# Kernel tuning notes

Hardware: AMD Instinct MI355X
Metric: run time of the kernel (lower is better)

## Reference

```python
import jax, jax.numpy as jnp
import numpy as np
import math

N, T, D_MODEL, H, D = 4, 2048, 1024, 16, 64


def setup_inputs() -> dict:
    key = jax.random.key(0)
    ks = jax.random.split(key, 12)
    s = 0.02
    return {
        "xq": jax.random.normal(ks[0], (N, T, D_MODEL), dtype=jnp.float32),
        "xk": jax.random.normal(ks[1], (N, T, D_MODEL), dtype=jnp.float32),
        "xv": jax.random.normal(ks[2], (N, T, D_MODEL), dtype=jnp.float32),
        "padding_mask": jnp.ones((N, T), dtype=jnp.int32),
        "Wq": jax.random.normal(ks[3], (D_MODEL, H * D), dtype=jnp.float32) * s,
        "bq": jnp.zeros((H * D,), dtype=jnp.float32),
        "Wk": jax.random.normal(ks[4], (D_MODEL, H * D), dtype=jnp.float32) * s,
        "bk": jnp.zeros((H * D,), dtype=jnp.float32),
        "Wv": jax.random.normal(ks[5], (D_MODEL, H * D), dtype=jnp.float32) * s,
        "bv": jnp.zeros((H * D,), dtype=jnp.float32),
        "Wo": jax.random.normal(ks[6], (H * D, D_MODEL), dtype=jnp.float32) * s,
        "bo": jnp.zeros((D_MODEL,), dtype=jnp.float32),
    }


def reference(xq, xk, xv, padding_mask, Wq, bq, Wk, bk, Wv, bv, Wo, bo):
    n, t_out, _ = xq.shape
    t_in = xk.shape[1]
    # projections
    Q = (xq @ Wq + bq).reshape(n, t_out, H, D).transpose(0, 2, 1, 3)  # [N,H,Tq,D]
    K = (xk @ Wk + bk).reshape(n, t_in, H, D).transpose(0, 2, 1, 3)   # [N,H,Tk,D]
    V = (xv @ Wv + bv).reshape(n, t_in, H, D).transpose(0, 2, 1, 3)
    scores = jnp.einsum("bhqd,bhkd->bhqk", Q, K) / math.sqrt(D)       # [N,H,Tq,Tk]
    neg_inf = jnp.float32(-jnp.inf)
    # padding mask: mask keys where padding_mask == 0
    scores = jnp.where(padding_mask[:, None, None, :] == 0, neg_inf, scores)
    # causal mask (tril of ones[max_len,max_len] sliced to [Tq,Tk])
    q_idx = jnp.arange(t_out)[:, None]
    k_idx = jnp.arange(t_in)[None, :]
    scores = jnp.where((k_idx <= q_idx)[None, None, :, :], scores, neg_inf)
    w = jax.nn.softmax(scores, axis=-1)
    attn = jnp.einsum("bhqk,bhkd->bhqd", w, V)                         # [N,H,Tq,D]
    attn = attn.transpose(0, 2, 1, 3).reshape(n, t_out, H * D)
    return attn @ Wo + bo
```

## Files before the change

### kernel.cpp

```cpp
#include <hip/hip_runtime.h>
#include <hip/hip_bf16.h>
#include <cstdint>

#define NB 4
#define TT 2048
#define DM 1024
#define NH 16
#define HD 64
#define QBLK 256
#define KVB 64

typedef __attribute__((ext_vector_type(8))) short bf16x8;
typedef __attribute__((ext_vector_type(4))) float f32x4;
typedef __attribute__((ext_vector_type(16))) float f32x16;
typedef __attribute__((ext_vector_type(4))) float float4v;
typedef __attribute__((ext_vector_type(4))) int i32x4;

static __device__ __forceinline__ unsigned short f2bf(float x) {
    unsigned int u = __float_as_uint(x);
    unsigned int r = (u + 0x7fffu + ((u >> 16) & 1u)) >> 16;
    return (unsigned short)r;
}
static __device__ __forceinline__ uint32_t pk2bf(float lo, float hi) {
    return (uint32_t)f2bf(lo) | ((uint32_t)f2bf(hi) << 16);
}

#define GLOAD16(gp, lp) __builtin_amdgcn_global_load_lds(                 \
    (const __attribute__((address_space(1))) void*)(gp),                  \
    (__attribute__((address_space(3))) void*)(lp), 16, 0, 0)
#define BAR() asm volatile("s_barrier" ::: "memory")
#define WAITV8() asm volatile("s_waitcnt vmcnt(8)" ::: "memory")
#define WAITV2() asm volatile("s_waitcnt vmcnt(2)" ::: "memory")
#define WAITV0() asm volatile("s_waitcnt vmcnt(0)" ::: "memory")

__global__ __launch_bounds__(256) void k_cvt3(const float* __restrict__ sq,
                                              const float* __restrict__ sk,
                                              const float* __restrict__ sv,
                                              unsigned short* __restrict__ dst,
                                              int n8) {
    const int z = blockIdx.y;
    const float* s = (z == 0) ? sq : (z == 1) ? sk : sv;
    unsigned short* d = dst + (size_t)z * n8 * 8;
    int i = blockIdx.x * 256 + threadIdx.x;
    const int stride = gridDim.x * 256;
    for (; i < n8; i += stride) {
        const float4v* sp = (const float4v*)(s + (size_t)i * 8);
        float4v v0 = sp[0], v1 = sp[1];
        uint4 o;
        o.x = pk2bf(v0[0], v0[1]);
        o.y = pk2bf(v0[2], v0[3]);
        o.z = pk2bf(v1[0], v1[1]);
        o.w = pk2bf(v1[2], v1[3]);
        *(uint4*)(d + (size_t)i * 8) = o;
    }
}

__global__ __launch_bounds__(256) void k_transpose_w(const float* __restrict__ W,
                                                     unsigned short* __restrict__ Wt) {
    __shared__ unsigned short tile[32][33];
    int tx = threadIdx.x, ty = threadIdx.y;
    int kb = blockIdx.x * 32, nb = blockIdx.y * 32;
#pragma unroll
    for (int i = 0; i < 4; ++i)
        tile[ty + i * 8][tx] = f2bf(W[(size_t)(kb + ty + i * 8) * DM + nb + tx]);
    __syncthreads();
#pragma unroll
    for (int i = 0; i < 4; ++i)
        Wt[(size_t)(nb + ty + i * 8) * DM + kb + tx] = tile[tx][ty + i * 8];
}

__global__ __launch_bounds__(256) void k_transpose_v(const unsigned short* __restrict__ V,
                                                     unsigned short* __restrict__ Vt) {
    __shared__ unsigned short tile[32][34];
    int tx = threadIdx.x, ty = threadIdx.y;
    int bh = blockIdx.z;
    int t0 = blockIdx.x * 32, d0 = blockIdx.y * 32;
    const unsigned short* src = V + (size_t)bh * TT * HD;
    unsigned short* dst = Vt + (size_t)bh * HD * TT;
#pragma unroll
    for (int i = 0; i < 4; ++i)
        tile[ty + i * 8][tx] = src[(size_t)(t0 + ty + i * 8) * HD + d0 + tx];
    __syncthreads();
#pragma unroll
    for (int i = 0; i < 4; ++i)
        dst[(size_t)(d0 + ty + i * 8) * TT + t0 + tx] = tile[tx][ty + i * 8];
}

template <int BATCHED>
__global__ __launch_bounds__(256) void k_gemm(const unsigned short* __restrict__ A0,
                                              const unsigned short* __restrict__ Bt0,
                                              const float* __restrict__ bias0,
                                              const float* __restrict__ bias1,
                                              const float* __restrict__ bias2,
                                              void* __restrict__ Cv, float scale0) {
    __shared__ __align__(16) char Asl[2][16384];
    __shared__ __align__(16) char Bsl[2][16384];
    const int tid = threadIdx.x;
    const int lane = tid & 63, wid = tid >> 6;
    const int lg = lane >> 4, lc = lane & 15;
    const int wm = wid >> 1, wn = wid & 1;
    const int m0 = blockIdx.x * 128, n0 = blockIdx.y * 128;
    const int z = BATCHED ? blockIdx.z : 0;

    const char* Ab = (const char*)(A0 + (size_t)z * NB * TT * DM);
    const char* Bb = (const char*)(Bt0 + (size_t)z * DM * DM);
    const float* bias = (z == 0) ? bias0 : (z == 1) ? bias1 : bias2;
    const float scale = (BATCHED && z != 0) ? 1.0f : scale0;

    f32x4 acc[4][4];
#pragma unroll
    for (int mi = 0; mi < 4; ++mi)
#pragma unroll
        for (int ni = 0; ni < 4; ++ni)
            acc[mi][ni] = (f32x4){0.f, 0.f, 0.f, 0.f};

    auto stage = [&](int buf, int k0) {
#pragma unroll
        for (int j = 0; j < 4; ++j) {
            const int row = j * 32 + (tid >> 3);
            const int swz = ((tid & 7) * 16) ^ ((row & 7) << 4);
            GLOAD16(Ab + (size_t)(m0 + row) * (DM * 2) + k0 * 2 + swz,
                    &Asl[buf][0] + j * 4096 + tid * 16);
            GLOAD16(Bb + (size_t)(n0 + row) * (DM * 2) + k0 * 2 + swz,
                    &Bsl[buf][0] + j * 4096 + tid * 16);
        }
    };

    stage(0, 0);
    __syncthreads();

    int cur = 0;
    for (int t = 0; t < DM / 64; ++t) {
        if (t + 1 < DM / 64) {
            stage(cur ^ 1, (t + 1) * 64);
            WAITV8();
        } else {
            WAITV0();
        }
        BAR();

#pragma unroll
        for (int kk = 0; kk < 2; ++kk) {
            bf16x8 af[4], bfr[4];
#pragma unroll
            for (int ni = 0; ni < 4; ++ni) {
                const int n = wn * 64 + ni * 16 + lc;
                bfr[ni] = *(const bf16x8*)(&Bsl[cur][0] + n * 128 +
                                           ((kk * 64 + lg * 16) ^ ((n & 7) << 4)));
            }
#pragma unroll
            for (int mi = 0; mi < 4; ++mi) {
                const int m = wm * 64 + mi * 16 + lc;
                af[mi] = *(const bf16x8*)(&Asl[cur][0] + m * 128 +
                                          ((kk * 64 + lg * 16) ^ ((m & 7) << 4)));
            }
            __builtin_amdgcn_s_setprio(1);
#pragma unroll
            for (int mi = 0; mi < 4; ++mi)
#pragma unroll
                for (int ni = 0; ni < 4; ++ni)
                    acc[mi][ni] = __builtin_amdgcn_mfma_f32_16x16x32_bf16(af[mi], bfr[ni],
                                                                          acc[mi][ni], 0, 0, 0);
            __builtin_amdgcn_s_setprio(0);
        }
        BAR();
        cur ^= 1;
    }

#pragma unroll
    for (int mi = 0; mi < 4; ++mi)
#pragma unroll
        for (int ni = 0; ni < 4; ++ni)
#pragma unroll
            for (int r = 0; r < 4; ++r) {
                int m = m0 + wm * 64 + mi * 16 + lg * 4 + r;
                int n = n0 + wn * 64 + ni * 16 + lc;
                float val = (acc[mi][ni][r] + bias[n]) * scale;
                if (BATCHED) {
                    int b = m >> 11, t = m & (TT - 1), h = n >> 6, d = n & 63;
                    ((unsigned short*)Cv)[(size_t)z * NB * NH * TT * HD +
                                          (((size_t)b * NH + h) * TT + t) * HD + d] = f2bf(val);
                } else {
                    ((float*)Cv)[(size_t)m * DM + n] = val;
                }
            }
}

__global__ __launch_bounds__(512) void k_attn(const unsigned short* __restrict__ Qg,
                                              const unsigned short* __restrict__ Kg,
                                              const unsigned short* __restrict__ Vtg,
                                              const int* __restrict__ pm,
                                              unsigned short* __restrict__ Og) {
    __shared__ __align__(16) unsigned short Kl[2][KVB * HD];
    __shared__ __align__(16) unsigned short Vl[2][KVB * HD];
    __shared__ uint64_t pmbits[TT / 64];

    const int idx = blockIdx.x;
    const int half = idx >> 8, r5 = idx & 255;
    const int a = r5 & 3;
    const int qb = half ? (7 - a) : a;
    const int bh = r5 >> 2;
    const int b = bh >> 4, h = bh & 15;
    const int qbase = qb * QBLK;
    const int tid = threadIdx.x;
    const int wid = tid >> 6, lane = tid & 63;
    const int hi = lane >> 5, l31 = lane & 31;
    const int q0 = qbase + wid * 32;
    const int q = q0 + l31;

    const unsigned short* Qh = Qg + (size_t)bh * TT * HD;
    const char* Khb = (const char*)(Kg + (size_t)bh * TT * HD);
    const char* Vthb = (const char*)(Vtg + (size_t)bh * HD * TT);
    const int* pmb = pm + b * TT;

    char* const kdst = (char*)&Kl[0][0];
    char* const vdst = (char*)&Vl[0][0];

    GLOAD16(Khb + (size_t)lane * 128 + wid * 16, kdst + tid * 16);
    GLOAD16(Vthb + (size_t)lane * 4096 + wid * 16, vdst + tid * 16);

#pragma unroll
    for (int it = 0; it < 4; ++it) {
        const int g = wid + it * 8;
        unsigned long long msk = __ballot(pmb[g * 64 + lane] != 0);
        if (lane == 0) pmbits[g] = msk;
    }

    bf16x8 qf[4];
#pragma unroll
    for (int dd = 0; dd < 4; ++dd)
        qf[dd] = *(const bf16x8*)((const char*)Qh + (size_t)q * 128 + dd * 32 + hi * 16);

    f32x16 o0, o1;
#pragma unroll
    for (int r = 0; r < 16; ++r) { o0[r] = 0.f; o1[r] = 0.f; }
    float mrow = -INFINITY, msafe = -1.0e30f, lrow = 0.f;

    __syncthreads();

    const int nt = (qbase + QBLK) >> 6;
    int cur = 0;
    for (int t = 0; t < nt; ++t) {
        const int kv0 = t << 6;
        if (t + 1 < nt) {
            const int kn = kv0 + KVB;
            const int nb = (cur ^ 1) * 8192 + tid * 16;
            GLOAD16(Khb + (size_t)(kn + lane) * 128 + wid * 16, kdst + nb);
            GLOAD16(Vthb + (size_t)lane * 4096 + (size_t)kn * 2 + wid * 16, vdst + nb);
            WAITV2();
        } else {
            WAITV0();
        }
        BAR();

        if (kv0 <= q0 + 31) {
            const uint64_t vb = pmbits[kv0 >> 6];
            const uint32_t pm0 = ((uint32_t)vb) >> (4 * hi);
            const uint32_t pm1 = ((uint32_t)(vb >> 32)) >> (4 * hi);
            const bool allvalid = (vb == ~0ull);
            const bool do2 = (kv0 + 32 <= q0 + 31);
            const bool needmask = (kv0 + 63 > q0) || !allvalid;
            const char* kb = (const char*)&Kl[0][0] + cur * 8192;
            const char* vbp = (const char*)&Vl[0][0] + cur * 8192;

            f32x16 st0, st1;
#pragma unroll
            for (int r = 0; r < 16; ++r) { st0[r] = 0.f; st1[r] = 0.f; }
            __builtin_amdgcn_s_setprio(1);
#pragma unroll
            for (int dd = 0; dd < 4; ++dd) {
                const char* kchunk = kb + (dd * 2 + hi) * 1024;
                bf16x8 kf = *(const bf16x8*)(kchunk + l31 * 16);
                st0 = __builtin_amdgcn_mfma_f32_32x32x16_bf16(kf, qf[dd], st0, 0, 0, 0);
            }
            if (do2) {
#pragma unroll
                for (int dd = 0; dd < 4; ++dd) {
                    const char* kchunk = kb + (dd * 2 + hi) * 1024;
                    bf16x8 kf = *(const bf16x8*)(kchunk + 512 + l31 * 16);
                    st1 = __builtin_amdgcn_mfma_f32_32x32x16_bf16(kf, qf[dd], st1, 0, 0, 0);
                }
            }
            __builtin_amdgcn_s_setprio(0);

            const int qr = q - kv0 - 4 * hi;
            if (needmask) {
#pragma unroll
                for (int r = 0; r < 16; ++r) {
                    const int c = (r & 3) + 8 * (r >> 2);
                    st0[r] = (((pm0 >> c) & 1) && (c <= qr)) ? st0[r] : -INFINITY;
                }
                if (do2) {
#pragma unroll
                    for (int r = 0; r < 16; ++r) {
                        const int c = (r & 3) + 8 * (r >> 2);
                        st1[r] = (((pm1 >> c) & 1) && (c + 32 <= qr)) ? st1[r] : -INFINITY;
                    }
                }
            }

            float mloc = -INFINITY;
#pragma unroll
            for (int r = 0; r < 16; ++r) mloc = fmaxf(mloc, st0[r]);
            if (do2) {
#pragma unroll
                for (int r = 0; r < 16; ++r) mloc = fmaxf(mloc, st1[r]);
            }
            const float cmax = fmaxf(mloc, __shfl_xor(mloc, 32, 64));
            if (!__all(cmax - mrow <= 8.0f)) {
                const float mnew = fmaxf(mrow, cmax);
                const float ms = fmaxf(mnew, -1.0e30f);
                const float esc = __builtin_amdgcn_exp2f(mrow - ms);
#pragma unroll
                for (int r = 0; r < 16; ++r) { o0[r] *= esc; o1[r] *= esc; }
                lrow *= esc;
                mrow = mnew;
                msafe = ms;
            }

            float tot = 0.f;
#pragma unroll
            for (int r = 0; r < 16; ++r) {
                st0[r] = __builtin_amdgcn_exp2f(st0[r] - msafe);
                tot += st0[r];
            }
            if (do2) {
#pragma unroll
                for (int r = 0; r < 16; ++r) {
                    st1[r] = __builtin_amdgcn_exp2f(st1[r] - msafe);
                    tot += st1[r];
                }
            }
            lrow += tot + __shfl_xor(tot, 32, 64);

            __builtin_amdgcn_s_setprio(1);
#pragma unroll
            for (int kc = 0; kc < 2; ++kc) {
                uint32_t A0 = pk2bf(st0[kc * 8 + 0], st0[kc * 8 + 1]);
                uint32_t A1 = pk2bf(st0[kc * 8 + 2], st0[kc * 8 + 3]);
                uint32_t C0 = pk2bf(st0[kc * 8 + 4], st0[kc * 8 + 5]);
                uint32_t C1 = pk2bf(st0[kc * 8 + 6], st0[kc * 8 + 7]);
                uint32_t oA0 = __shfl_xor(A0, 32, 64), oA1 = __shfl_xor(A1, 32, 64);
                uint32_t oC0 = __shfl_xor(C0, 32, 64), oC1 = __shfl_xor(C1, 32, 64);
                i32x4 pf = {(int)(hi ? oC0 : A0), (int)(hi ? oC1 : A1),
                            (int)(hi ? C0 : oA0), (int)(hi ? C1 : oA1)};
                bf16x8 pb = *(bf16x8*)&pf;
                const char* vchunk = vbp + (kc * 2 + hi) * 1024;
                {
                    bf16x8 vf = *(const bf16x8*)(vchunk + l31 * 16);
                    o0 = __builtin_amdgcn_mfma_f32_32x32x16_bf16(vf, pb, o0, 0, 0, 0);
                }
                {
                    bf16x8 vf = *(const bf16x8*)(vchunk + 512 + l31 * 16);
                    o1 = __builtin_amdgcn_mfma_f32_32x32x16_bf16(vf, pb, o1, 0, 0, 0);
                }
            }
            if (do2) {
#pragma unroll
                for (int kc = 0; kc < 2; ++kc) {
                    uint32_t A0 = pk2bf(st1[kc * 8 + 0], st1[kc * 8 + 1]);
                    uint32_t A1 = pk2bf(st1[kc * 8 + 2], st1[kc * 8 + 3]);
                    uint32_t C0 = pk2bf(st1[kc * 8 + 4], st1[kc * 8 + 5]);
                    uint32_t C1 = pk2bf(st1[kc * 8 + 6], st1[kc * 8 + 7]);
                    uint32_t oA0 = __shfl_xor(A0, 32, 64), oA1 = __shfl_xor(A1, 32, 64);
                    uint32_t oC0 = __shfl_xor(C0, 32, 64), oC1 = __shfl_xor(C1, 32, 64);
                    i32x4 pf = {(int)(hi ? oC0 : A0), (int)(hi ? oC1 : A1),
                                (int)(hi ? C0 : oA0), (int)(hi ? C1 : oA1)};
                    bf16x8 pb = *(bf16x8*)&pf;
                    const char* vchunk = vbp + (4 + kc * 2 + hi) * 1024;
                    {
                        bf16x8 vf = *(const bf16x8*)(vchunk + l31 * 16);
                        o0 = __builtin_amdgcn_mfma_f32_32x32x16_bf16(vf, pb, o0, 0, 0, 0);
                    }
                    {
                        bf16x8 vf = *(const bf16x8*)(vchunk + 512 + l31 * 16);
                        o1 = __builtin_amdgcn_mfma_f32_32x32x16_bf16(vf, pb, o1, 0, 0, 0);
                    }
                }
            }
            __builtin_amdgcn_s_setprio(0);
        }
        BAR();
        cur ^= 1;
    }

    const float inv = (lrow > 0.f) ? (1.0f / lrow) : 0.f;
    unsigned short* orow = Og + ((size_t)(b * TT + q)) * DM + h * HD;
#pragma unroll
    for (int g4 = 0; g4 < 4; ++g4) {
        uint32_t w0 = pk2bf(o0[g4 * 4 + 0] * inv, o0[g4 * 4 + 1] * inv);
        uint32_t w1 = pk2bf(o0[g4 * 4 + 2] * inv, o0[g4 * 4 + 3] * inv);
        *(uint2*)(orow + g4 * 8 + 4 * hi) = make_uint2(w0, w1);
    }
#pragma unroll
    for (int g4 = 0; g4 < 4; ++g4) {
        uint32_t w0 = pk2bf(o1[g4 * 4 + 0] * inv, o1[g4 * 4 + 1] * inv);
        uint32_t w1 = pk2bf(o1[g4 * 4 + 2] * inv, o1[g4 * 4 + 3] * inv);
        *(uint2*)(orow + 32 + g4 * 8 + 4 * hi) = make_uint2(w0, w1);
    }
}

extern "C" void kernel_launch(void* const* d_in, const int* in_sizes, int n_in,
                              void* d_out, int out_size, void* d_ws, size_t ws_size,
                              hipStream_t stream) {
    const float* xq = (const float*)d_in[0];
    const float* xk = (const float*)d_in[1];
    const float* xv = (const float*)d_in[2];
    const int* pmask = (const int*)d_in[3];
    const float* Wq = (const float*)d_in[4];
    const float* bq = (const float*)d_in[5];
    const float* Wk = (const float*)d_in[6];
    const float* bk = (const float*)d_in[7];
    const float* Wv = (const float*)d_in[8];
    const float* bv = (const float*)d_in[9];
    const float* Wo = (const float*)d_in[10];
    const float* bo = (const float*)d_in[11];

    char* ws = (char*)d_ws;
    const size_t WT = (size_t)DM * DM * 2;
    const size_t QKV = (size_t)NB * NH * TT * HD * 2;
    unsigned short* WqT = (unsigned short*)(ws + 0 * WT);
    unsigned short* WoT = (unsigned short*)(ws + 3 * WT);
    unsigned short* Qb = (unsigned short*)(ws + 4 * WT);
    unsigned short* Kb = (unsigned short*)(ws + 4 * WT + QKV);
    unsigned short* Vb = (unsigned short*)(ws + 4 * WT + 2 * QKV);
    unsigned short* Vt = (unsigned short*)(ws + 4 * WT + 3 * QKV);
    unsigned short* Xb = (unsigned short*)(ws + 4 * WT + 4 * QKV);
    unsigned short* Ob = Vb;

    dim3 tb(32, 8);
    k_transpose_w<<<dim3(32, 32), tb, 0, stream>>>(Wq, WqT);
    k_transpose_w<<<dim3(32, 32), tb, 0, stream>>>(Wk, WqT + DM * DM);
    k_transpose_w<<<dim3(32, 32), tb, 0, stream>>>(Wv, WqT + 2 * DM * DM);
    k_transpose_w<<<dim3(32, 32), tb, 0, stream>>>(Wo, WoT);

    const float qscale = 0.125f * 1.44269504088896340736f;
    const int n8 = NB * TT * DM / 8;

    k_cvt3<<<dim3(1024, 3), 256, 0, stream>>>(xq, xk, xv, Xb, n8);
    k_gemm<1><<<dim3(64, 8, 3), 256, 0, stream>>>(Xb, WqT, bq, bk, bv, Qb, qscale);

    k_transpose_v<<<dim3(TT / 32, HD / 32, NB * NH), tb, 0, stream>>>(Vb, Vt);

    k_attn<<<dim3((TT / QBLK) * NB * NH), 512, 0, stream>>>(Qb, Kb, Vt, pmask, Ob);

    k_gemm<0><<<dim3(64, 8, 1), 256, 0, stream>>>(Ob, WoT, bo, bo, bo, d_out, 1.0f);
}
```

Before: 216.6 us.

## Fuse fp32-to-bf16 input conversion and V transpose into QKV projection GEMM

The QKV GEMM now loads fp32 activations directly through registers, converts them to bf16 and writes them into swizzled LDS. This removes the separate conversion kernel and its bf16 round trip through global memory. The V projection epilogue writes straight into the transposed layout, so the separate V transpose kernel is dropped. In exchange the A operand no longer uses async global-to-LDS loads, and register-staged conversion adds VALU work and register pressure inside the GEMM main loop.

```diff
diff --git a/kernel.cpp b/kernel.cpp
--- a/kernel.cpp
+++ b/kernel.cpp
@@ -22,38 +22,20 @@
     return (unsigned short)r;
 }
 static __device__ __forceinline__ uint32_t pk2bf(float lo, float hi) {
-    return (uint32_t)f2bf(lo) | ((uint32_t)f2bf(hi) << 16);
+    union { __hip_bfloat162 v; uint32_t u; } c;
+    c.v = __float22bfloat162_rn(float2{lo, hi});
+    return c.u;
 }
 
 #define GLOAD16(gp, lp) __builtin_amdgcn_global_load_lds(                 \
     (const __attribute__((address_space(1))) void*)(gp),                  \
     (__attribute__((address_space(3))) void*)(lp), 16, 0, 0)
 #define BAR() asm volatile("s_barrier" ::: "memory")
+#define LGKM0() asm volatile("s_waitcnt lgkmcnt(0)" ::: "memory")
 #define WAITV8() asm volatile("s_waitcnt vmcnt(8)" ::: "memory")
+#define WAITV4() asm volatile("s_waitcnt vmcnt(4)" ::: "memory")
 #define WAITV2() asm volatile("s_waitcnt vmcnt(2)" ::: "memory")
 #define WAITV0() asm volatile("s_waitcnt vmcnt(0)" ::: "memory")
-
-__global__ __launch_bounds__(256) void k_cvt3(const float* __restrict__ sq,
-                                              const float* __restrict__ sk,
-                                              const float* __restrict__ sv,
-                                              unsigned short* __restrict__ dst,
-                                              int n8) {
-    const int z = blockIdx.y;
-    const float* s = (z == 0) ? sq : (z == 1) ? sk : sv;
-    unsigned short* d = dst + (size_t)z * n8 * 8;
-    int i = blockIdx.x * 256 + threadIdx.x;
-    const int stride = gridDim.x * 256;
-    for (; i < n8; i += stride) {
-        const float4v* sp = (const float4v*)(s + (size_t)i * 8);
-        float4v v0 = sp[0], v1 = sp[1];
-        uint4 o;
-        o.x = pk2bf(v0[0], v0[1]);
-        o.y = pk2bf(v0[2], v0[3]);
-        o.z = pk2bf(v1[0], v1[1]);
-        o.w = pk2bf(v1[2], v1[3]);
-        *(uint4*)(d + (size_t)i * 8) = o;
-    }
-}
 
 __global__ __launch_bounds__(256) void k_transpose_w(const float* __restrict__ W,
                                                      unsigned short* __restrict__ Wt) {
@@ -69,30 +51,16 @@
         Wt[(size_t)(nb + ty + i * 8) * DM + kb + tx] = tile[tx][ty + i * 8];
 }
 
-__global__ __launch_bounds__(256) void k_transpose_v(const unsigned short* __restrict__ V,
-                                                     unsigned short* __restrict__ Vt) {
-    __shared__ unsigned short tile[32][34];
-    int tx = threadIdx.x, ty = threadIdx.y;
-    int bh = blockIdx.z;
-    int t0 = blockIdx.x * 32, d0 = blockIdx.y * 32;
-    const unsigned short* src = V + (size_t)bh * TT * HD;
-    unsigned short* dst = Vt + (size_t)bh * HD * TT;
-#pragma unroll
-    for (int i = 0; i < 4; ++i)
-        tile[ty + i * 8][tx] = src[(size_t)(t0 + ty + i * 8) * HD + d0 + tx];
-    __syncthreads();
-#pragma unroll
-    for (int i = 0; i < 4; ++i)
-        dst[(size_t)(d0 + ty + i * 8) * TT + t0 + tx] = tile[tx][ty + i * 8];
-}
-
-template <int BATCHED>
-__global__ __launch_bounds__(256) void k_gemm(const unsigned short* __restrict__ A0,
-                                              const unsigned short* __restrict__ Bt0,
-                                              const float* __restrict__ bias0,
-                                              const float* __restrict__ bias1,
-                                              const float* __restrict__ bias2,
-                                              void* __restrict__ Cv, float scale0) {
+__global__ __launch_bounds__(256) void k_gemm_qkv(const float* __restrict__ xq,
+                                                  const float* __restrict__ xk,
+                                                  const float* __restrict__ xv,
+                                                  const unsigned short* __restrict__ Wt3,
+                                                  const float* __restrict__ bq,
+                                                  const float* __restrict__ bk,
+                                                  const float* __restrict__ bv,
+                                                  unsigned short* __restrict__ QKb,
+                                                  unsigned short* __restrict__ Vt,
+                                                  float qscale) {
     __shared__ __align__(16) char Asl[2][16384];
     __shared__ __align__(16) char Bsl[2][16384];
     const int tid = threadIdx.x;
@@ -100,12 +68,138 @@
     const int lg = lane >> 4, lc = lane & 15;
     const int wm = wid >> 1, wn = wid & 1;
     const int m0 = blockIdx.x * 128, n0 = blockIdx.y * 128;
-    const int z = BATCHED ? blockIdx.z : 0;
-
-    const char* Ab = (const char*)(A0 + (size_t)z * NB * TT * DM);
-    const char* Bb = (const char*)(Bt0 + (size_t)z * DM * DM);
-    const float* bias = (z == 0) ? bias0 : (z == 1) ? bias1 : bias2;
-    const float scale = (BATCHED && z != 0) ? 1.0f : scale0;
+    const int z = blockIdx.z;
+
+    const float* Af = (z == 0) ? xq : (z == 1) ? xk : xv;
+    const char* Bb = (const char*)(Wt3 + (size_t)z * DM * DM);
+    const float* bias = (z == 0) ? bq : (z == 1) ? bk : bv;
+    const float scale = (z == 0) ? qscale : 1.0f;
+
+    const int arow = tid >> 1, ahalf = tid & 1;
+    float4v areg[8];
+
+    auto issueA = [&](int k0) {
+        const float4v* p = (const float4v*)(Af + (size_t)(m0 + arow) * DM + k0 + ahalf * 32);
+#pragma unroll
+        for (int j = 0; j < 8; ++j) areg[j] = p[j];
+    };
+    auto writeA = [&](int buf) {
+        char* base = &Asl[buf][0] + arow * 128;
+        const int x = (arow & 7) << 4;
+#pragma unroll
+        for (int j = 0; j < 4; ++j) {
+            uint4 w;
+            w.x = pk2bf(areg[2 * j][0], areg[2 * j][1]);
+            w.y = pk2bf(areg[2 * j][2], areg[2 * j][3]);
+            w.z = pk2bf(areg[2 * j + 1][0], areg[2 * j + 1][1]);
+            w.w = pk2bf(areg[2 * j + 1][2], areg[2 * j + 1][3]);
+            *(uint4*)(base + ((ahalf * 64 + j * 16) ^ x)) = w;
+        }
+    };
+    auto issueB = [&](int buf, int k0) {
+#pragma unroll
+        for (int j = 0; j < 4; ++j) {
+            const int row = j * 32 + (tid >> 3);
+            const int swz = ((tid & 7) * 16) ^ ((row & 7) << 4);
+            GLOAD16(Bb + (size_t)(n0 + row) * (DM * 2) + k0 * 2 + swz,
+                    &Bsl[buf][0] + j * 4096 + tid * 16);
+        }
+    };
+
+    f32x4 acc[4][4];
+#pragma unroll
+    for (int mi = 0; mi < 4; ++mi)
+#pragma unroll
+        for (int ni = 0; ni < 4; ++ni)
+            acc[mi][ni] = (f32x4){0.f, 0.f, 0.f, 0.f};
+
+    issueA(0);
+    issueB(0, 0);
+    WAITV4();
+    writeA(0);
+    issueA(64);
+    LGKM0();
+    WAITV8();
+    BAR();
+
+    int cur = 0;
+    for (int t = 0; t < 16; ++t) {
+        if (t < 15) issueB(cur ^ 1, (t + 1) * 64);
+
+#pragma unroll
+        for (int kk = 0; kk < 2; ++kk) {
+            bf16x8 af[4], bfr[4];
+#pragma unroll
+            for (int ni = 0; ni < 4; ++ni) {
+                const int n = wn * 64 + ni * 16 + lc;
+                bfr[ni] = *(const bf16x8*)(&Bsl[cur][0] + n * 128 +
+                                           ((kk * 64 + lg * 16) ^ ((n & 7) << 4)));
+            }
+#pragma unroll
+            for (int mi = 0; mi < 4; ++mi) {
+                const int m = wm * 64 + mi * 16 + lc;
+                af[mi] = *(const bf16x8*)(&Asl[cur][0] + m * 128 +
+                                          ((kk * 64 + lg * 16) ^ ((m & 7) << 4)));
+            }
+            __builtin_amdgcn_s_setprio(1);
+#pragma unroll
+            for (int mi = 0; mi < 4; ++mi)
+#pragma unroll
+                for (int ni = 0; ni < 4; ++ni)
+                    acc[mi][ni] = __builtin_amdgcn_mfma_f32_16x16x32_bf16(af[mi], bfr[ni],
+                                                                          acc[mi][ni], 0, 0, 0);
+            __builtin_amdgcn_s_setprio(0);
+        }
+
+        if (t < 15) {
+            WAITV4();
+            writeA(cur ^ 1);
+            if (t < 14) issueA((t + 2) * 64);
+            LGKM0();
+            if (t < 14) { WAITV8(); } else { WAITV0(); }
+            BAR();
+            cur ^= 1;
+        }
+    }
+
+#pragma unroll
+    for (int mi = 0; mi < 4; ++mi)
+#pragma unroll
+        for (int ni = 0; ni < 4; ++ni) {
+            const int m = m0 + wm * 64 + mi * 16 + lg * 4;
+            const int n = n0 + wn * 64 + ni * 16 + lc;
+            float v[4];
+#pragma unroll
+            for (int r = 0; r < 4; ++r) v[r] = (acc[mi][ni][r] + bias[n]) * scale;
+            const int b = m >> 11, tl = m & (TT - 1), h = n >> 6, d = n & 63;
+            if (z == 2) {
+                uint2 w;
+                w.x = pk2bf(v[0], v[1]);
+                w.y = pk2bf(v[2], v[3]);
+                *(uint2*)(Vt + ((size_t)(b * NH + h) * HD + d) * TT + tl) = w;
+            } else {
+#pragma unroll
+                for (int r = 0; r < 4; ++r)
+                    QKb[(size_t)z * NB * NH * TT * HD +
+                        (((size_t)b * NH + h) * TT + tl + r) * HD + d] = f2bf(v[r]);
+            }
+        }
+}
+
+__global__ __launch_bounds__(256) void k_gemm_o(const unsigned short* __restrict__ A,
+                                                const unsigned short* __restrict__ Bt,
+                                                const float* __restrict__ bias,
+                                                float* __restrict__ C) {
+    __shared__ __align__(16) char Asl[2][16384];
+    __shared__ __align__(16) char Bsl[2][16384];
+    const int tid = threadIdx.x;
+    const int lane = tid & 63, wid = tid >> 6;
+    const int lg = lane >> 4, lc = lane & 15;
+    const int wm = wid >> 1, wn = wid & 1;
+    const int m0 = blockIdx.x * 128, n0 = blockIdx.y * 128;
+
+    const char* Ab = (const char*)A;
+    const char* Bb = (const char*)Bt;
 
     f32x4 acc[4][4];
 #pragma unroll
@@ -175,14 +269,7 @@
             for (int r = 0; r < 4; ++r) {
                 int m = m0 + wm * 64 + mi * 16 + lg * 4 + r;
                 int n = n0 + wn * 64 + ni * 16 + lc;
-                float val = (acc[mi][ni][r] + bias[n]) * scale;
-                if (BATCHED) {
-                    int b = m >> 11, t = m & (TT - 1), h = n >> 6, d = n & 63;
-                    ((unsigned short*)Cv)[(size_t)z * NB * NH * TT * HD +
-                                          (((size_t)b * NH + h) * TT + t) * HD + d] = f2bf(val);
-                } else {
-                    ((float*)Cv)[(size_t)m * DM + n] = val;
-                }
+                C[(size_t)m * DM + n] = acc[mi][ni][r] + bias[n];
             }
 }
 
@@ -423,10 +510,8 @@
     unsigned short* WoT = (unsigned short*)(ws + 3 * WT);
     unsigned short* Qb = (unsigned short*)(ws + 4 * WT);
     unsigned short* Kb = (unsigned short*)(ws + 4 * WT + QKV);
-    unsigned short* Vb = (unsigned short*)(ws + 4 * WT + 2 * QKV);
-    unsigned short* Vt = (unsigned short*)(ws + 4 * WT + 3 * QKV);
-    unsigned short* Xb = (unsigned short*)(ws + 4 * WT + 4 * QKV);
-    unsigned short* Ob = Vb;
+    unsigned short* Vt = (unsigned short*)(ws + 4 * WT + 2 * QKV);
+    unsigned short* Ob = (unsigned short*)(ws + 4 * WT + 3 * QKV);
 
     dim3 tb(32, 8);
     k_transpose_w<<<dim3(32, 32), tb, 0, stream>>>(Wq, WqT);
@@ -435,14 +520,11 @@
     k_transpose_w<<<dim3(32, 32), tb, 0, stream>>>(Wo, WoT);
 
     const float qscale = 0.125f * 1.44269504088896340736f;
-    const int n8 = NB * TT * DM / 8;
-
-    k_cvt3<<<dim3(1024, 3), 256, 0, stream>>>(xq, xk, xv, Xb, n8);
-    k_gemm<1><<<dim3(64, 8, 3), 256, 0, stream>>>(Xb, WqT, bq, bk, bv, Qb, qscale);
-
-    k_transpose_v<<<dim3(TT / 32, HD / 32, NB * NH), tb, 0, stream>>>(Vb, Vt);
+
+    k_gemm_qkv<<<dim3(64, 8, 3), 256, 0, stream>>>(xq, xk, xv, WqT, bq, bk, bv,
+                                                   Qb, Vt, qscale);
 
     k_attn<<<dim3((TT / QBLK) * NB * NH), 512, 0, stream>>>(Qb, Kb, Vt, pmask, Ob);
 
-    k_gemm<0><<<dim3(64, 8, 1), 256, 0, stream>>>(Ob, WoT, bo, bo, bo, d_out, 1.0f);
-}
+    k_gemm_o<<<dim3(64, 8), 256, 0, stream>>>(Ob, WoT, bo, (float*)d_out);
+}
```

Result: slower. 246.0 us (+13.6%).
